# Kernel optimization log

Hardware: AMD Instinct MI355X
Metric: run time of the kernel (lower is better)

Reference implementation:

```python
import jax, jax.numpy as jnp
import numpy as np

B, T, C, H = 4, 2048, 1024, 16
HS = C // H  # head_size = 64


def setup_inputs() -> dict:
    key = jax.random.key(0)
    ks = jax.random.split(key, 12)
    s_in = C ** -0.5
    s_ff = (4 * C) ** -0.5
    return {
        "x": jax.random.normal(ks[0], (B, T, C), jnp.float32),
        "Wq": jax.random.normal(ks[1], (H, C, HS), jnp.float32) * s_in,
        "Wk": jax.random.normal(ks[2], (H, C, HS), jnp.float32) * s_in,
        "Wv": jax.random.normal(ks[3], (H, C, HS), jnp.float32) * s_in,
        "Wp": jax.random.normal(ks[4], (C, C), jnp.float32) * s_in,
        "bp": jnp.zeros((C,), jnp.float32),
        "W1": jax.random.normal(ks[5], (C, 4 * C), jnp.float32) * s_in,
        "b1": jnp.zeros((4 * C,), jnp.float32),
        "W2": jax.random.normal(ks[6], (4 * C, C), jnp.float32) * s_ff,
        "b2": jnp.zeros((C,), jnp.float32),
        "g1": jnp.ones((C,), jnp.float32),
        "be1": jnp.zeros((C,), jnp.float32),
        "g2": jnp.ones((C,), jnp.float32),
        "be2": jnp.zeros((C,), jnp.float32),
    }


def _layernorm(x, g, b, eps=1e-5):
    mu = jnp.mean(x, axis=-1, keepdims=True)
    var = jnp.var(x, axis=-1, keepdims=True)
    return (x - mu) * jax.lax.rsqrt(var + eps) * g + b


def reference(x, Wq, Wk, Wv, Wp, bp, W1, b1, W2, b2, g1, be1, g2, be2):
    # NOTE: residuals add to the post-LN tensor (faithful to the torch code),
    # and the attention scale uses C = n_embed, not head_size.
    x1 = _layernorm(x, g1, be1)                       # [B,T,C]
    q = jnp.einsum('btc,hcd->bhtd', x1, Wq)
    k = jnp.einsum('btc,hcd->bhtd', x1, Wk)
    v = jnp.einsum('btc,hcd->bhtd', x1, Wv)
    scores = jnp.einsum('bhtd,bhsd->bhts', q, k) * (C ** -0.5)
    causal = jnp.tril(jnp.ones((T, T), bool))
    scores = jnp.where(causal, scores, -jnp.inf)
    att = jax.nn.softmax(scores, axis=-1)             # [B,H,T,T]
    o = jnp.einsum('bhts,bhsd->bhtd', att, v)
    o = o.transpose(0, 2, 1, 3).reshape(B, T, C)      # concat heads
    x2 = x1 + o @ Wp + bp
    x3 = _layernorm(x2, g2, be2)
    ff = jax.nn.relu(x3 @ W1 + b1) @ W2 + b2
    return x3 + ff
```

## Files before the change

### kernel.cpp

```cpp
#include <hip/hip_runtime.h>
#include <cstdint>

typedef unsigned short u16;
typedef unsigned int u32;
typedef __bf16 bf16x8 __attribute__((ext_vector_type(8)));
typedef float f32x4 __attribute__((ext_vector_type(4)));

#define DEVINL __device__ __forceinline__

DEVINL float bf2f(u16 h) { union { u32 u; float f; } v; v.u = ((u32)h) << 16; return v.f; }
DEVINL u16 f2bf(float f) {
  union { float f; u32 u; } v; v.f = f;
  u32 u = v.u;
  return (u16)((u + 0x7fffu + ((u >> 16) & 1u)) >> 16);
}

DEVINL float fexp2(float x) {
#if __has_builtin(__builtin_amdgcn_exp2f)
  return __builtin_amdgcn_exp2f(x);
#else
  return exp2f(x);
#endif
}

DEVINL void gld_lds16(const void* g, void* l) {
  __builtin_amdgcn_global_load_lds(
      (__attribute__((address_space(1))) void*)(g),
      (__attribute__((address_space(3))) void*)(l), 16, 0, 0);
}

__global__ __launch_bounds__(256) void ktransf(const float* __restrict__ in,
                                               u16* __restrict__ out,
                                               int R, int C, long ibs, long obs) {
  __shared__ __align__(16) u16 tile[64][80];
  const float* ip = in + (long)blockIdx.z * ibs;
  u16* op = out + (long)blockIdx.z * obs;
  int c0 = blockIdx.x * 64, r0 = blockIdx.y * 64;
  int t = threadIdx.x;
#pragma unroll
  for (int ph = 0; ph < 2; ++ph) {
    int ch = ph * 256 + t;
    int r = ch >> 3, cc = (ch & 7) * 8;
    const float* src = &ip[(long)(r0 + r) * C + c0 + cc];
    float4 a = *(const float4*)src;
    float4 b = *(const float4*)(src + 4);
    u16 tmp[8] = {f2bf(a.x), f2bf(a.y), f2bf(a.z), f2bf(a.w),
                  f2bf(b.x), f2bf(b.y), f2bf(b.z), f2bf(b.w)};
    *(uint4*)&tile[r][cc] = *(uint4*)tmp;
  }
  __syncthreads();
#pragma unroll
  for (int ph = 0; ph < 2; ++ph) {
    int ch = ph * 256 + t;
    int c = ch >> 3, rr = (ch & 7) * 8;
    u16 tmp[8];
#pragma unroll
    for (int i = 0; i < 8; ++i) tmp[i] = tile[rr + i][c];
    *(uint4*)&op[(long)(c0 + c) * R + r0 + rr] = *(uint4*)tmp;
  }
}

__global__ __launch_bounds__(256) void kln_f(const float* __restrict__ x,
                                             const float* __restrict__ g,
                                             const float* __restrict__ be,
                                             u16* __restrict__ y) {
  long row = blockIdx.x;
  int t = threadIdx.x;
  float4 xv = *(const float4*)&x[row * 1024 + t * 4];
  float f0 = xv.x, f1 = xv.y, f2 = xv.z, f3 = xv.w;
  float s = f0 + f1 + f2 + f3;
  float s2 = f0 * f0 + f1 * f1 + f2 * f2 + f3 * f3;
#pragma unroll
  for (int off = 32; off >= 1; off >>= 1) {
    s += __shfl_xor(s, off);
    s2 += __shfl_xor(s2, off);
  }
  __shared__ float red[8];
  int w = t >> 6, l = t & 63;
  if (l == 0) { red[w] = s; red[4 + w] = s2; }
  __syncthreads();
  s = red[0] + red[1] + red[2] + red[3];
  s2 = red[4] + red[5] + red[6] + red[7];
  float mu = s * (1.0f / 1024.0f);
  float var = s2 * (1.0f / 1024.0f) - mu * mu;
  float rs = rsqrtf(var + 1e-5f);
  float4 gv = *(const float4*)&g[t * 4];
  float4 bv = *(const float4*)&be[t * 4];
  ushort4 ov;
  ov.x = f2bf((f0 - mu) * rs * gv.x + bv.x);
  ov.y = f2bf((f1 - mu) * rs * gv.y + bv.y);
  ov.z = f2bf((f2 - mu) * rs * gv.z + bv.z);
  ov.w = f2bf((f3 - mu) * rs * gv.w + bv.w);
  *(ushort4*)&y[row * 1024 + t * 4] = ov;
}

__global__ __launch_bounds__(256) void kln_b(const u16* __restrict__ x,
                                             const float* __restrict__ g,
                                             const float* __restrict__ be,
                                             u16* __restrict__ y) {
  long row = blockIdx.x;
  int t = threadIdx.x;
  ushort4 xv = *(const ushort4*)&x[row * 1024 + t * 4];
  float f0 = bf2f(xv.x), f1 = bf2f(xv.y), f2 = bf2f(xv.z), f3 = bf2f(xv.w);
  float s = f0 + f1 + f2 + f3;
  float s2 = f0 * f0 + f1 * f1 + f2 * f2 + f3 * f3;
#pragma unroll
  for (int off = 32; off >= 1; off >>= 1) {
    s += __shfl_xor(s, off);
    s2 += __shfl_xor(s2, off);
  }
  __shared__ float red[8];
  int w = t >> 6, l = t & 63;
  if (l == 0) { red[w] = s; red[4 + w] = s2; }
  __syncthreads();
  s = red[0] + red[1] + red[2] + red[3];
  s2 = red[4] + red[5] + red[6] + red[7];
  float mu = s * (1.0f / 1024.0f);
  float var = s2 * (1.0f / 1024.0f) - mu * mu;
  float rs = rsqrtf(var + 1e-5f);
  float4 gv = *(const float4*)&g[t * 4];
  float4 bv = *(const float4*)&be[t * 4];
  ushort4 ov;
  ov.x = f2bf((f0 - mu) * rs * gv.x + bv.x);
  ov.y = f2bf((f1 - mu) * rs * gv.y + bv.y);
  ov.z = f2bf((f2 - mu) * rs * gv.z + bv.z);
  ov.w = f2bf((f3 - mu) * rs * gv.w + bv.w);
  *(ushort4*)&y[row * 1024 + t * 4] = ov;
}

template <int EPI, int OF32>
__global__ __launch_bounds__(256) void kgemm(const u16* __restrict__ A,
                                             const u16* __restrict__ BT, int K,
                                             const float* __restrict__ bias,
                                             const u16* __restrict__ resid,
                                             void* __restrict__ outv, int ldc,
                                             u16* __restrict__ vout) {
  __shared__ __align__(16) u16 sA[128 * 64];
  __shared__ __align__(16) u16 sB[128 * 64];
  int tid = threadIdx.x;
  int l = tid & 63, wv = tid >> 6;
  int wm = (wv >> 1) * 64, wn = (wv & 1) * 64;
  long m0 = (long)blockIdx.y * 128, n0 = (long)blockIdx.x * 128;
  const u16* Ab = A + m0 * K;
  const u16* Bb = BT + n0 * K;
  f32x4 acc[4][4] = {};

  for (int k0 = 0; k0 < K; k0 += 64) {
    __syncthreads();
#pragma unroll
    for (int it = 0; it < 4; ++it) {
      int c = it * 256 + tid;
      int r = c >> 3;
      int k8 = (c & 7) ^ (r & 7);
      gld_lds16(Ab + (long)r * K + k0 + k8 * 8, &sA[c * 8]);
    }
#pragma unroll
    for (int it = 0; it < 4; ++it) {
      int c = it * 256 + tid;
      int r = c >> 3;
      int k8 = (c & 7) ^ (r & 7);
      gld_lds16(Bb + (long)r * K + k0 + k8 * 8, &sB[c * 8]);
    }
    __syncthreads();
#pragma unroll
    for (int kk = 0; kk < 2; ++kk) {
      int k8 = kk * 4 + (l >> 4);
      bf16x8 af[4], bfr[4];
#pragma unroll
      for (int mi = 0; mi < 4; ++mi) {
        int r = wm + mi * 16 + (l & 15);
        af[mi] = *(const bf16x8*)&sA[(r * 8 + (k8 ^ (r & 7))) * 8];
      }
#pragma unroll
      for (int ni = 0; ni < 4; ++ni) {
        int r = wn + ni * 16 + (l & 15);
        bfr[ni] = *(const bf16x8*)&sB[(r * 8 + (k8 ^ (r & 7))) * 8];
      }
#pragma unroll
      for (int mi = 0; mi < 4; ++mi)
#pragma unroll
        for (int ni = 0; ni < 4; ++ni)
          acc[mi][ni] =
              __builtin_amdgcn_mfma_f32_16x16x32_bf16(af[mi], bfr[ni], acc[mi][ni], 0, 0, 0);
    }
  }
#pragma unroll
  for (int mi = 0; mi < 4; ++mi) {
#pragma unroll
    for (int ni = 0; ni < 4; ++ni) {
#pragma unroll
      for (int j = 0; j < 4; ++j) {
        long row = m0 + wm + mi * 16 + (l >> 4) * 4 + j;
        long col = n0 + wn + ni * 16 + (l & 15);
        float v = acc[mi][ni][j];
        if constexpr (EPI == 0) {
          long tn = col >> 10, jj = col & 1023;
          long hh = jj >> 6, dd = jj & 63;
          long bb = row >> 11, tt = row & 2047;
          if (tn == 0) {
            v *= 0.045084220027780106f;
            ((u16*)outv)[(((bb)*16 + hh) * 2048 + tt) * 64 + dd] = f2bf(v);
          } else if (tn == 1) {
            ((u16*)outv)[(((4 + bb) * 16 + hh) * 2048 + tt) * 64 + dd] = f2bf(v);
          } else {
            vout[((bb * 16 + hh) * 64 + dd) * 2048 + tt] = f2bf(v);
          }
        } else {
          v += bias[col];
          if constexpr (EPI == 2) v = fmaxf(v, 0.0f);
          if constexpr (EPI == 1) v += bf2f(resid[row * ldc + col]);
          if constexpr (OF32) ((float*)outv)[row * ldc + col] = v;
          else ((u16*)outv)[row * ldc + col] = f2bf(v);
        }
      }
    }
  }
}

__global__ __launch_bounds__(256) void kattn(const u16* __restrict__ q,
                                             const u16* __restrict__ kmat,
                                             const u16* __restrict__ vt,
                                             u16* __restrict__ o) {
  __shared__ __align__(16) u16 Ks[64 * 64];
  __shared__ __align__(16) u16 Vs[64 * 64];
  __shared__ __align__(16) u16 Ps[4 * 32 * 64];
  int bh = blockIdx.x;
  int qi = (gridDim.y - 1) - blockIdx.y;
  int tid = threadIdx.x, w = tid >> 6, l = tid & 63;
  long bQ = (long)bh * 2048 * 64;
  int qrow0 = qi * 128 + w * 32;
  const float NEGINF = -__builtin_inff();

  bf16x8 qf[2][2];
#pragma unroll
  for (int mi = 0; mi < 2; ++mi)
#pragma unroll
    for (int kk = 0; kk < 2; ++kk) {
      int tt = qrow0 + mi * 16 + (l & 15);
      int kd = kk * 32 + (l >> 4) * 8;
      qf[mi][kk] = *(const bf16x8*)&q[bQ + (long)tt * 64 + kd];
    }
  f32x4 ao[2][4] = {};
  float mr[2][4], lr[2][4];
#pragma unroll
  for (int mi = 0; mi < 2; ++mi)
#pragma unroll
    for (int j = 0; j < 4; ++j) { mr[mi][j] = NEGINF; lr[mi][j] = 0.f; }

  u16* Pw = &Ps[w * 2048];
  int njt = qi * 2 + 2;
  for (int jt = 0; jt < njt; ++jt) {
    int s0 = jt * 64;
    bool skip = (s0 > qrow0 + 31);
    bool need_mask = (s0 + 63 > qrow0);
    __syncthreads();
#pragma unroll
    for (int it = 0; it < 2; ++it) {
      int c = it * 256 + tid;
      int r = c >> 3;
      int k8 = (c & 7) ^ (r & 7);
      gld_lds16(&kmat[bQ + (long)(s0 + r) * 64 + k8 * 8], &Ks[c * 8]);
    }
#pragma unroll
    for (int it = 0; it < 2; ++it) {
      int c = it * 256 + tid;
      int r = c >> 3;
      int s8 = (c & 7) ^ (r & 7);
      gld_lds16(&vt[bQ + (long)r * 2048 + s0 + s8 * 8], &Vs[c * 8]);
    }
    __syncthreads();
    if (skip) continue;
    f32x4 sc[2][4] = {};
#pragma unroll
    for (int kk = 0; kk < 2; ++kk) {
      int k8 = kk * 4 + (l >> 4);
      bf16x8 kf[4];
#pragma unroll
      for (int ni = 0; ni < 4; ++ni) {
        int r = ni * 16 + (l & 15);
        kf[ni] = *(const bf16x8*)&Ks[(r * 8 + (k8 ^ (r & 7))) * 8];
      }
#pragma unroll
      for (int mi = 0; mi < 2; ++mi)
#pragma unroll
        for (int ni = 0; ni < 4; ++ni)
          sc[mi][ni] =
              __builtin_amdgcn_mfma_f32_16x16x32_bf16(qf[mi][kk], kf[ni], sc[mi][ni], 0, 0, 0);
    }
#pragma unroll
    for (int mi = 0; mi < 2; ++mi) {
#pragma unroll
      for (int j = 0; j < 4; ++j) {
        int tg = qrow0 + mi * 16 + (l >> 4) * 4 + j;
        float rmax = NEGINF;
        if (need_mask) {
#pragma unroll
          for (int ni = 0; ni < 4; ++ni) {
            int sg = s0 + ni * 16 + (l & 15);
            float vv = sc[mi][ni][j];
            vv = (sg <= tg) ? vv : NEGINF;
            sc[mi][ni][j] = vv;
            rmax = fmaxf(rmax, vv);
          }
        } else {
#pragma unroll
          for (int ni = 0; ni < 4; ++ni) rmax = fmaxf(rmax, sc[mi][ni][j]);
        }
#pragma unroll
        for (int off = 8; off >= 1; off >>= 1) rmax = fmaxf(rmax, __shfl_xor(rmax, off));
        float mnew = fmaxf(mr[mi][j], rmax);
        float alpha = fexp2(mr[mi][j] - mnew);
        float rsum = 0.f;
#pragma unroll
        for (int ni = 0; ni < 4; ++ni) {
          float p = fexp2(sc[mi][ni][j] - mnew);
          sc[mi][ni][j] = p;
          rsum += p;
        }
#pragma unroll
        for (int off = 8; off >= 1; off >>= 1) rsum += __shfl_xor(rsum, off);
        lr[mi][j] = lr[mi][j] * alpha + rsum;
        mr[mi][j] = mnew;
#pragma unroll
        for (int nd = 0; nd < 4; ++nd) ao[mi][nd][j] *= alpha;
      }
    }
#pragma unroll
    for (int mi = 0; mi < 2; ++mi)
#pragma unroll
      for (int ni = 0; ni < 4; ++ni)
#pragma unroll
        for (int j = 0; j < 4; ++j) {
          int r = mi * 16 + (l >> 4) * 4 + j;
          int cc = ni * 16 + (l & 15);
          Pw[(r * 8 + ((cc >> 3) ^ (r & 7))) * 8 + (cc & 7)] = f2bf(sc[mi][ni][j]);
        }
#pragma unroll
    for (int kk = 0; kk < 2; ++kk) {
      int s8 = kk * 4 + (l >> 4);
      bf16x8 pf[2], vf[4];
#pragma unroll
      for (int mi = 0; mi < 2; ++mi) {
        int r = mi * 16 + (l & 15);
        pf[mi] = *(const bf16x8*)&Pw[(r * 8 + (s8 ^ (r & 7))) * 8];
      }
#pragma unroll
      for (int nd = 0; nd < 4; ++nd) {
        int r = nd * 16 + (l & 15);
        vf[nd] = *(const bf16x8*)&Vs[(r * 8 + (s8 ^ (r & 7))) * 8];
      }
#pragma unroll
      for (int mi = 0; mi < 2; ++mi)
#pragma unroll
        for (int nd = 0; nd < 4; ++nd)
          ao[mi][nd] =
              __builtin_amdgcn_mfma_f32_16x16x32_bf16(pf[mi], vf[nd], ao[mi][nd], 0, 0, 0);
    }
  }
  int b = bh >> 4, h = bh & 15;
#pragma unroll
  for (int mi = 0; mi < 2; ++mi)
#pragma unroll
    for (int nd = 0; nd < 4; ++nd)
#pragma unroll
      for (int j = 0; j < 4; ++j) {
        int tt = qrow0 + mi * 16 + (l >> 4) * 4 + j;
        int dd = nd * 16 + (l & 15);
        float v = ao[mi][nd][j] / lr[mi][j];
        o[((long)(b * 2048 + tt)) * 1024 + h * 64 + dd] = f2bf(v);
      }
}

extern "C" void kernel_launch(void* const* d_in, const int* in_sizes, int n_in,
                              void* d_out, int out_size, void* d_ws, size_t ws_size,
                              hipStream_t stream) {
  const float* x = (const float*)d_in[0];
  const float* Wq = (const float*)d_in[1];
  const float* Wk = (const float*)d_in[2];
  const float* Wv = (const float*)d_in[3];
  const float* Wp = (const float*)d_in[4];
  const float* bp = (const float*)d_in[5];
  const float* W1 = (const float*)d_in[6];
  const float* b1 = (const float*)d_in[7];
  const float* W2 = (const float*)d_in[8];
  const float* b2 = (const float*)d_in[9];
  const float* g1 = (const float*)d_in[10];
  const float* be1 = (const float*)d_in[11];
  const float* g2 = (const float*)d_in[12];
  const float* be2 = (const float*)d_in[13];

  u16* ws = (u16*)d_ws;
  u16* wqkvT = ws;
  u16* wpT = wqkvT + 3145728;
  u16* w1T = wpT + 1048576;
  u16* w2T = w1T + 4194304;
  u16* qb = w2T + 4194304;
  u16* kb = qb + 8388608;
  u16* vb = kb + 8388608;
  u16* vtb = vb + 8388608;
  u16* ob = vtb + 8388608;
  u16* x1 = ob + 8388608;
  float* outp = (float*)d_out;
  u16* x2 = vb;
  u16* x3 = ob;
  u16* hb = qb;

  ktransf<<<dim3(1, 16, 16), 256, 0, stream>>>(Wq, wqkvT, 1024, 64, 65536, 65536);
  ktransf<<<dim3(1, 16, 16), 256, 0, stream>>>(Wk, wqkvT + 1048576, 1024, 64, 65536, 65536);
  ktransf<<<dim3(1, 16, 16), 256, 0, stream>>>(Wv, wqkvT + 2097152, 1024, 64, 65536, 65536);
  ktransf<<<dim3(16, 16, 1), 256, 0, stream>>>(Wp, wpT, 1024, 1024, 0, 0);
  ktransf<<<dim3(64, 16, 1), 256, 0, stream>>>(W1, w1T, 1024, 4096, 0, 0);
  ktransf<<<dim3(16, 64, 1), 256, 0, stream>>>(W2, w2T, 4096, 1024, 0, 0);

  kln_f<<<8192, 256, 0, stream>>>(x, g1, be1, x1);
  kgemm<0, 0><<<dim3(24, 64), 256, 0, stream>>>(x1, wqkvT, 1024, nullptr, nullptr, qb, 0, vtb);
  kattn<<<dim3(64, 16), 256, 0, stream>>>(qb, kb, vtb, ob);
  kgemm<1, 0><<<dim3(8, 64), 256, 0, stream>>>(ob, wpT, 1024, bp, x1, x2, 1024, nullptr);
  kln_b<<<8192, 256, 0, stream>>>(x2, g2, be2, x3);
  kgemm<2, 0><<<dim3(32, 64), 256, 0, stream>>>(x3, w1T, 1024, b1, nullptr, hb, 4096, nullptr);
  kgemm<1, 1><<<dim3(8, 64), 256, 0, stream>>>(hb, w2T, 4096, b2, x3, outp, 1024, nullptr);
}
```

Measured before the change: 466.3 us.

## Add 256x256 8-wave pipelined GEMM for the FFN up-projection

Replaces the generic GEMM for the W1 + bias + ReLU step with a new kernel using 512-thread blocks and 256x256 output tiles, double-buffered LDS with XOR swizzle, and stage loads interleaved across four compute phases with barriers and s_setprio around MFMA bursts. The larger tile is meant to raise operand reuse, and the interleaved direct-to-LDS loads are meant to overlap global traffic with MFMA work. In exchange it uses 128KB of LDS and many accumulator registers per block, which limits occupancy. It also gives a smaller grid (512 blocks), which may balance poorly across CUs.

```diff
diff --git a/kernel.cpp b/kernel.cpp
--- a/kernel.cpp
+++ b/kernel.cpp
@@ -217,6 +217,136 @@
   }
 }
 
+#define KG8_READB()                                                          \
+  _Pragma("unroll") for (int ni = 0; ni < 4; ++ni)                           \
+      _Pragma("unroll") for (int kk = 0; kk < 2; ++kk) {                     \
+    int r = wc * 64 + ni * 16 + (l & 15);                                    \
+    int s = (kk * 4 + (l >> 4)) ^ (r & 7);                                   \
+    bfr[ni][kk] = *(const bf16x8*)&sB[cur][(r * 8 + s) * 8];                 \
+  }
+#define KG8_PHASE(qq)                                                        \
+  {                                                                          \
+    bf16x8 afr[2][2];                                                        \
+    _Pragma("unroll") for (int mi = 0; mi < 2; ++mi)                         \
+        _Pragma("unroll") for (int kk = 0; kk < 2; ++kk) {                   \
+      int r = wr * 128 + (qq)*32 + mi * 16 + (l & 15);                       \
+      int s = (kk * 4 + (l >> 4)) ^ (r & 7);                                 \
+      afr[mi][kk] = *(const bf16x8*)&sA[cur][(r * 8 + s) * 8];               \
+    }                                                                        \
+    __builtin_amdgcn_s_setprio(1);                                          \
+    _Pragma("unroll") for (int kk = 0; kk < 2; ++kk)                         \
+        _Pragma("unroll") for (int mi = 0; mi < 2; ++mi)                     \
+            _Pragma("unroll") for (int ni = 0; ni < 4; ++ni)                 \
+                acc[(qq)*2 + mi][ni] =                                       \
+                    __builtin_amdgcn_mfma_f32_16x16x32_bf16(                 \
+                        afr[mi][kk], bfr[ni][kk], acc[(qq)*2 + mi][ni],      \
+                        0, 0, 0);                                            \
+    __builtin_amdgcn_s_setprio(0);                                          \
+  }
+#define KG8_BAR()                 \
+  __builtin_amdgcn_sched_barrier(0); \
+  __builtin_amdgcn_s_barrier();
+
+__global__ __launch_bounds__(512, 2) void kgemm8(const u16* __restrict__ A,
+                                                 const u16* __restrict__ BT,
+                                                 int K,
+                                                 const float* __restrict__ bias,
+                                                 u16* __restrict__ out, int ldc) {
+  __shared__ __align__(16) u16 sA[2][256 * 64];
+  __shared__ __align__(16) u16 sB[2][256 * 64];
+  int tid = threadIdx.x;
+  int w = tid >> 6, l = tid & 63;
+  int wr = w >> 2, wc = w & 3;
+  long m0 = (long)blockIdx.y * 256, n0 = (long)blockIdx.x * 256;
+  const u16* Ab = A + m0 * K;
+  const u16* Bb = BT + n0 * K;
+  int nt = K >> 6;
+  f32x4 acc[8][4] = {};
+
+  auto stageA = [&](int b, int t, int p) {
+    int ri = tid >> 3;
+    int r = (ri < 32) ? (p * 32 + ri) : (128 + p * 32 + (ri - 32));
+    int s = tid & 7;
+    int k8 = s ^ (r & 7);
+    int chunk = (ri < 32) ? (p * 256 + tid) : (1024 + p * 256 + (tid - 256));
+    gld_lds16(Ab + (long)r * K + t * 64 + k8 * 8, &sA[b][chunk * 8]);
+  };
+  auto stageB = [&](int b, int t, int p) {
+    int r = p * 64 + (tid >> 3);
+    int s = tid & 7;
+    int k8 = s ^ (r & 7);
+    gld_lds16(Bb + (long)r * K + t * 64 + k8 * 8, &sB[b][(p * 512 + tid) * 8]);
+  };
+
+#pragma unroll
+  for (int p = 0; p < 4; ++p) { stageA(0, 0, p); stageB(0, 0, p); }
+#pragma unroll
+  for (int p = 0; p < 3; ++p) { stageA(1, 1, p); stageB(1, 1, p); }
+  asm volatile("s_waitcnt vmcnt(6)" ::: "memory");
+  KG8_BAR();
+
+  for (int t = 0; t + 2 < nt; ++t) {
+    const int cur = t & 1;
+    const int nxt = cur ^ 1;
+    bf16x8 bfr[4][2];
+    stageA(nxt, t + 1, 3);
+    stageB(nxt, t + 1, 3);
+    KG8_READB();
+    KG8_PHASE(0);
+    KG8_BAR();
+    stageA(cur, t + 2, 0);
+    stageB(cur, t + 2, 0);
+    KG8_PHASE(1);
+    KG8_BAR();
+    stageA(cur, t + 2, 1);
+    stageB(cur, t + 2, 1);
+    KG8_PHASE(2);
+    KG8_BAR();
+    stageA(cur, t + 2, 2);
+    stageB(cur, t + 2, 2);
+    KG8_PHASE(3);
+    asm volatile("s_waitcnt vmcnt(6)" ::: "memory");
+    KG8_BAR();
+  }
+  {
+    const int cur = (nt - 2) & 1;
+    const int nxt = cur ^ 1;
+    stageA(nxt, nt - 1, 3);
+    stageB(nxt, nt - 1, 3);
+    bf16x8 bfr[4][2];
+    KG8_READB();
+    KG8_PHASE(0);
+    KG8_PHASE(1);
+    KG8_PHASE(2);
+    KG8_PHASE(3);
+    asm volatile("s_waitcnt vmcnt(0)" ::: "memory");
+    KG8_BAR();
+  }
+  {
+    const int cur = (nt - 1) & 1;
+    bf16x8 bfr[4][2];
+    KG8_READB();
+    KG8_PHASE(0);
+    KG8_PHASE(1);
+    KG8_PHASE(2);
+    KG8_PHASE(3);
+  }
+#pragma unroll
+  for (int m8 = 0; m8 < 8; ++m8) {
+#pragma unroll
+    for (int ni = 0; ni < 4; ++ni) {
+#pragma unroll
+      for (int j = 0; j < 4; ++j) {
+        long row = m0 + wr * 128 + m8 * 16 + (l >> 4) * 4 + j;
+        long col = n0 + wc * 64 + ni * 16 + (l & 15);
+        float v = acc[m8][ni][j] + bias[col];
+        v = fmaxf(v, 0.0f);
+        out[row * (long)ldc + col] = f2bf(v);
+      }
+    }
+  }
+}
+
 __global__ __launch_bounds__(256) void kattn(const u16* __restrict__ q,
                                              const u16* __restrict__ kmat,
                                              const u16* __restrict__ vt,
@@ -417,6 +547,6 @@
   kattn<<<dim3(64, 16), 256, 0, stream>>>(qb, kb, vtb, ob);
   kgemm<1, 0><<<dim3(8, 64), 256, 0, stream>>>(ob, wpT, 1024, bp, x1, x2, 1024, nullptr);
   kln_b<<<8192, 256, 0, stream>>>(x2, g2, be2, x3);
-  kgemm<2, 0><<<dim3(32, 64), 256, 0, stream>>>(x3, w1T, 1024, b1, nullptr, hb, 4096, nullptr);
+  kgemm8<<<dim3(16, 32), 512, 0, stream>>>(x3, w1T, 1024, b1, hb, 4096);
   kgemm<1, 1><<<dim3(8, 64), 256, 0, stream>>>(hb, w2T, 4096, b2, x3, outp, 1024, nullptr);
 }
```

Measured after the change: 481.5 us. 3.3% more time.
